# Kernel optimization log

Hardware: AMD Instinct MI355X
Metric: run time of the kernel (lower is better)

Reference implementation:

```python
import jax, jax.numpy as jnp
import numpy as np

N = 40000
E = 640000
D_IN = 128
D_OUT = 128
LN_EPS = 1e-5
LEAKY_ALPHA = 0.2


def setup_inputs() -> dict:
    key = jax.random.key(0)
    ks = jax.random.split(key, 8)
    x = jax.random.normal(ks[0], (N, D_IN), dtype=jnp.float32)
    edge_index = jax.random.randint(ks[1], (2, E), 0, N, dtype=jnp.int64)
    edge_weight = jax.random.uniform(ks[2], (E,), dtype=jnp.float32)
    # learned parameters (kaiming-uniform-ish init for weight)
    bound_w = np.sqrt(6.0 / D_IN) / np.sqrt(1.0 + 5.0)
    weight = jax.random.uniform(ks[3], (D_IN, D_OUT), minval=-bound_w, maxval=bound_w, dtype=jnp.float32)
    adaptive_weight = jax.random.uniform(ks[4], (1,), dtype=jnp.float32)
    bound_b = 1.0 / np.sqrt(D_IN)
    bias = jax.random.uniform(ks[5], (D_OUT,), minval=-bound_b, maxval=bound_b, dtype=jnp.float32)
    ln_gamma = jnp.ones((D_OUT,), dtype=jnp.float32)
    ln_beta = jnp.zeros((D_OUT,), dtype=jnp.float32)
    return {"x": x, "edge_index": edge_index, "edge_weight": edge_weight,
            "weight": weight, "adaptive_weight": adaptive_weight, "bias": bias,
            "ln_gamma": ln_gamma, "ln_beta": ln_beta}


def reference(x, edge_index, edge_weight, weight, adaptive_weight, bias, ln_gamma, ln_beta):
    n = x.shape[0]
    out = x @ weight  # [N, D_OUT]
    row, col = edge_index[0], edge_index[1]
    aew = edge_weight * jax.nn.sigmoid(adaptive_weight[0])  # [E]
    # degree via scatter_add over row
    deg = jax.ops.segment_sum(aew, row, num_segments=n)  # [N]
    deg_inv_sqrt = jnp.where(deg > 0, deg ** -0.5, 0.0)
    norm = deg_inv_sqrt[row] * aew * deg_inv_sqrt[col]  # [E]
    # gather-scale-scatter propagate
    out = jax.ops.segment_sum(out[col] * norm[:, None], row, num_segments=n)  # [N, D_OUT]
    out = out + bias
    # LayerNorm over feature dim
    mu = jnp.mean(out, axis=-1, keepdims=True)
    var = jnp.mean((out - mu) ** 2, axis=-1, keepdims=True)
    out = (out - mu) * jax.lax.rsqrt(var + LN_EPS) * ln_gamma + ln_beta
    # LeakyReLU
    out = jnp.where(out >= 0, out, LEAKY_ALPHA * out)
    return out
```

## Files before the change

kernel.cpp:

```cpp
#include <hip/hip_runtime.h>
#include <hip/hip_bf16.h>
#include <math.h>

#define N_NODES 40000
#define E_EDGES 640000
#define D 128
#define LN_EPS 1e-5f
#define LEAKY 0.2f
#define NB 157

__global__ __launch_bounds__(256) void k_zero(int* __restrict__ cnt) {
    int i = blockIdx.x * 256 + threadIdx.x;
    if (i < N_NODES) cnt[i] = 0;
}

#define BM 32
__global__ __launch_bounds__(256) void k_gemm(const float* __restrict__ x,
                                              const float* __restrict__ w,
                                              float* __restrict__ out) {
    __shared__ float ws[128 * 128];
    __shared__ float xs[BM * 128];
    int t = threadIdx.x;

    const float4* w4 = (const float4*)w;
    float4* ws4 = (float4*)ws;
#pragma unroll
    for (int i = 0; i < 16; i++) ws4[t + i * 256] = w4[t + i * 256];

    int row0 = blockIdx.x * BM;
    const float4* x4 = (const float4*)(x + (size_t)row0 * D);
    float4* xs4 = (float4*)xs;
#pragma unroll
    for (int i = 0; i < 4; i++) xs4[t + i * 256] = x4[t + i * 256];

    __syncthreads();

    int c0 = (t & 31) * 4;
    int r0 = (t >> 5) * 4;
    float acc[4][4] = {};
#pragma unroll 4
    for (int k = 0; k < 128; k++) {
        float4 wv = *(const float4*)&ws[k * 128 + c0];
        float x0 = xs[(r0 + 0) * 128 + k];
        float x1 = xs[(r0 + 1) * 128 + k];
        float x2 = xs[(r0 + 2) * 128 + k];
        float x3 = xs[(r0 + 3) * 128 + k];
        acc[0][0] += x0 * wv.x; acc[0][1] += x0 * wv.y; acc[0][2] += x0 * wv.z; acc[0][3] += x0 * wv.w;
        acc[1][0] += x1 * wv.x; acc[1][1] += x1 * wv.y; acc[1][2] += x1 * wv.z; acc[1][3] += x1 * wv.w;
        acc[2][0] += x2 * wv.x; acc[2][1] += x2 * wv.y; acc[2][2] += x2 * wv.z; acc[2][3] += x2 * wv.w;
        acc[3][0] += x3 * wv.x; acc[3][1] += x3 * wv.y; acc[3][2] += x3 * wv.z; acc[3][3] += x3 * wv.w;
    }
#pragma unroll
    for (int i = 0; i < 4; i++) {
        int row = row0 + r0 + i;
        *(float4*)&out[(size_t)row * D + c0] =
            make_float4(acc[i][0], acc[i][1], acc[i][2], acc[i][3]);
    }
}

__global__ __launch_bounds__(256) void k_cnt(const int* __restrict__ ei,
                                             int* __restrict__ cnt,
                                             int* __restrict__ rank) {
    int e = blockIdx.x * 256 + threadIdx.x;
    if (e >= E_EDGES) return;
    rank[e] = atomicAdd(&cnt[ei[e]], 1);
}

__global__ __launch_bounds__(256) void k_scanA(const int* __restrict__ cnt,
                                               int* __restrict__ bsum) {
    __shared__ int red[256];
    int t = threadIdx.x;
    int i = blockIdx.x * 256 + t;
    red[t] = (i < N_NODES) ? cnt[i] : 0;
    __syncthreads();
    for (int off = 128; off > 0; off >>= 1) {
        if (t < off) red[t] += red[t + off];
        __syncthreads();
    }
    if (t == 0) bsum[blockIdx.x] = red[0];
}

__global__ __launch_bounds__(256) void k_scanB(const int* __restrict__ bsum,
                                               int* __restrict__ boff,
                                               int* __restrict__ rowstart) {
    __shared__ int s[256];
    int t = threadIdx.x;
    int v = (t < NB) ? bsum[t] : 0;
    s[t] = v;
    __syncthreads();
    for (int off = 1; off < 256; off <<= 1) {
        int u = (t >= off) ? s[t - off] : 0;
        __syncthreads();
        s[t] += u;
        __syncthreads();
    }
    if (t < NB) boff[t] = s[t] - v;
    if (t == 0) rowstart[N_NODES] = E_EDGES;
}

__global__ __launch_bounds__(256) void k_scanC(const int* __restrict__ cnt,
                                               const int* __restrict__ boff,
                                               int* __restrict__ rowstart) {
    __shared__ int s[256];
    int t = threadIdx.x;
    int i = blockIdx.x * 256 + t;
    int v = (i < N_NODES) ? cnt[i] : 0;
    s[t] = v;
    __syncthreads();
    for (int off = 1; off < 256; off <<= 1) {
        int u = (t >= off) ? s[t - off] : 0;
        __syncthreads();
        s[t] += u;
        __syncthreads();
    }
    if (i < N_NODES) rowstart[i] = boff[blockIdx.x] + s[t] - v;
}

__global__ __launch_bounds__(256) void k_scat(const int* __restrict__ ei,
                                              const float* __restrict__ ew,
                                              const float* __restrict__ aw,
                                              const int* __restrict__ rowstart,
                                              const int* __restrict__ rank,
                                              float2* __restrict__ srec) {
    int e = blockIdx.x * 256 + threadIdx.x;
    if (e >= E_EDGES) return;
    float sig = 1.f / (1.f + __expf(-aw[0]));
    int r = ei[e];
    int c = ei[E_EDGES + e];
    int slot = rowstart[r] + rank[e];
    srec[slot] = make_float2(__int_as_float(c), ew[e] * sig);
}

__global__ __launch_bounds__(256) void k_degdis(const int* __restrict__ rowstart,
                                                const float2* __restrict__ srec,
                                                float* __restrict__ dis) {
    int i = blockIdx.x * 256 + threadIdx.x;
    if (i >= N_NODES) return;
    int s = rowstart[i];
    int e = rowstart[i + 1];
    float d = 0.f;
    for (int j = s; j < e; j++) d += srec[j].y;
    dis[i] = (d > 0.f) ? rsqrtf(d) : 0.f;
}

__global__ __launch_bounds__(256) void k_agg(const int* __restrict__ rowstart,
                                             const float2* __restrict__ srec,
                                             const float* __restrict__ out_lin,
                                             const float* __restrict__ dis,
                                             const float* __restrict__ bias,
                                             const float* __restrict__ gamma,
                                             const float* __restrict__ beta,
                                             float* __restrict__ out) {
    int w = (blockIdx.x * 256 + threadIdx.x) >> 6;
    int lane = threadIdx.x & 63;
    if (w >= N_NODES) return;
    int s = __builtin_amdgcn_readfirstlane(rowstart[w]);
    int e = __builtin_amdgcn_readfirstlane(rowstart[w + 1]);
    float dr = dis[w];

    float2 acc = make_float2(0.f, 0.f);
    for (int i = s; i < e; i++) {
        float2 rec = srec[i];
        int c = __float_as_int(rec.x);
        float v = rec.y * dis[c];
        const float2 t = *(const float2*)&out_lin[(size_t)c * D + lane * 2];
        acc.x += t.x * v;
        acc.y += t.y * v;
    }
    acc.x *= dr; acc.y *= dr;

    float2 b = *(const float2*)&bias[lane * 2];
    acc.x += b.x; acc.y += b.y;

    float sm = acc.x + acc.y;
#pragma unroll
    for (int m = 1; m < 64; m <<= 1) sm += __shfl_xor(sm, m);
    float mu = sm * (1.f / 128.f);

    float dx = acc.x - mu, dy = acc.y - mu;
    float q = dx * dx + dy * dy;
#pragma unroll
    for (int m = 1; m < 64; m <<= 1) q += __shfl_xor(q, m);
    float rstd = rsqrtf(q * (1.f / 128.f) + LN_EPS);

    float2 g  = *(const float2*)&gamma[lane * 2];
    float2 be = *(const float2*)&beta[lane * 2];
    float y0 = dx * rstd * g.x + be.x;
    float y1 = dy * rstd * g.y + be.y;
    y0 = (y0 >= 0.f) ? y0 : LEAKY * y0;
    y1 = (y1 >= 0.f) ? y1 : LEAKY * y1;
    *(float2*)&out[(size_t)w * D + lane * 2] = make_float2(y0, y1);
}

extern "C" void kernel_launch(void* const* d_in, const int* in_sizes, int n_in,
                              void* d_out, int out_size, void* d_ws, size_t ws_size,
                              hipStream_t stream) {
    const float* x      = (const float*)d_in[0];
    const int*   ei     = (const int*)d_in[1];
    const float* ew     = (const float*)d_in[2];
    const float* w      = (const float*)d_in[3];
    const float* aw     = (const float*)d_in[4];
    const float* bias   = (const float*)d_in[5];
    const float* gamma  = (const float*)d_in[6];
    const float* beta   = (const float*)d_in[7];
    float* out = (float*)d_out;

    char* p = (char*)d_ws;
    float* out_lin  = (float*)p;            p += (size_t)N_NODES * D * 4;
    float* dis      = (float*)p;            p += N_NODES * 4;
    int*   cnt      = (int*)p;              p += N_NODES * 4;
    int*   rowstart = (int*)p;              p += (N_NODES + 1) * 4;
    int*   rank     = (int*)p;              p += (size_t)E_EDGES * 4;
    int*   bsum     = (int*)p;              p += NB * 4;
    int*   boff     = (int*)p;              p += NB * 4;
    float2* srec    = (float2*)((((uintptr_t)p) + 15) & ~(uintptr_t)15);

    k_zero<<<NB, 256, 0, stream>>>(cnt);
    k_gemm<<<N_NODES / BM, 256, 0, stream>>>(x, w, out_lin);
    k_cnt<<<(E_EDGES + 255) / 256, 256, 0, stream>>>(ei, cnt, rank);
    k_scanA<<<NB, 256, 0, stream>>>(cnt, bsum);
    k_scanB<<<1, 256, 0, stream>>>(bsum, boff, rowstart);
    k_scanC<<<NB, 256, 0, stream>>>(cnt, boff, rowstart);
    k_scat<<<(E_EDGES + 255) / 256, 256, 0, stream>>>(ei, ew, aw, rowstart, rank, srec);
    k_degdis<<<NB, 256, 0, stream>>>(rowstart, srec, dis);
    k_agg<<<(N_NODES + 3) / 4, 256, 0, stream>>>(rowstart, srec, out_lin, dis,
                                                 bias, gamma, beta, out);
}
```

Measured before the change: 215.4 us.

## Store linear output in bf16 and fold counter zeroing into GEMM

The GEMM now writes its output as bf16 instead of fp32, which halves the bytes the aggregation kernel gathers per edge from random rows. The separate zeroing kernel is removed and the count zeroing is folded into the GEMM kernel's first threads, saving one launch. This trades precision in the intermediate features (bf16 rounding before accumulation) for lower gather bandwidth, which may affect tolerance.

```diff
diff --git a/kernel.cpp b/kernel.cpp
--- a/kernel.cpp
+++ b/kernel.cpp
@@ -9,15 +9,14 @@
 #define LEAKY 0.2f
 #define NB 157
 
-__global__ __launch_bounds__(256) void k_zero(int* __restrict__ cnt) {
-    int i = blockIdx.x * 256 + threadIdx.x;
-    if (i < N_NODES) cnt[i] = 0;
-}
-
 #define BM 32
 __global__ __launch_bounds__(256) void k_gemm(const float* __restrict__ x,
                                               const float* __restrict__ w,
-                                              float* __restrict__ out) {
+                                              __hip_bfloat16* __restrict__ outb,
+                                              int* __restrict__ cnt) {
+    int gid = blockIdx.x * 256 + threadIdx.x;
+    if (gid < N_NODES) cnt[gid] = 0;
+
     __shared__ float ws[128 * 128];
     __shared__ float xs[BM * 128];
     int t = threadIdx.x;
@@ -53,8 +52,12 @@
 #pragma unroll
     for (int i = 0; i < 4; i++) {
         int row = row0 + r0 + i;
-        *(float4*)&out[(size_t)row * D + c0] =
-            make_float4(acc[i][0], acc[i][1], acc[i][2], acc[i][3]);
+        __hip_bfloat162 p0 = __float22bfloat162_rn(make_float2(acc[i][0], acc[i][1]));
+        __hip_bfloat162 p1 = __float22bfloat162_rn(make_float2(acc[i][2], acc[i][3]));
+        uint2 pk;
+        pk.x = *(unsigned int*)&p0;
+        pk.y = *(unsigned int*)&p1;
+        *(uint2*)&outb[(size_t)row * D + c0] = pk;
     }
 }
 
@@ -145,7 +148,7 @@
 
 __global__ __launch_bounds__(256) void k_agg(const int* __restrict__ rowstart,
                                              const float2* __restrict__ srec,
-                                             const float* __restrict__ out_lin,
+                                             const __hip_bfloat162* __restrict__ lin2,
                                              const float* __restrict__ dis,
                                              const float* __restrict__ bias,
                                              const float* __restrict__ gamma,
@@ -163,9 +166,10 @@
         float2 rec = srec[i];
         int c = __float_as_int(rec.x);
         float v = rec.y * dis[c];
-        const float2 t = *(const float2*)&out_lin[(size_t)c * D + lane * 2];
-        acc.x += t.x * v;
-        acc.y += t.y * v;
+        __hip_bfloat162 t = lin2[(size_t)c * 64 + lane];
+        float2 tf = __bfloat1622float2(t);
+        acc.x += tf.x * v;
+        acc.y += tf.y * v;
     }
     acc.x *= dr; acc.y *= dr;
 
@@ -206,7 +210,7 @@
     float* out = (float*)d_out;
 
     char* p = (char*)d_ws;
-    float* out_lin  = (float*)p;            p += (size_t)N_NODES * D * 4;
+    __hip_bfloat16* out_lin = (__hip_bfloat16*)p; p += (size_t)N_NODES * D * 2;
     float* dis      = (float*)p;            p += N_NODES * 4;
     int*   cnt      = (int*)p;              p += N_NODES * 4;
     int*   rowstart = (int*)p;              p += (N_NODES + 1) * 4;
@@ -215,14 +219,14 @@
     int*   boff     = (int*)p;              p += NB * 4;
     float2* srec    = (float2*)((((uintptr_t)p) + 15) & ~(uintptr_t)15);
 
-    k_zero<<<NB, 256, 0, stream>>>(cnt);
-    k_gemm<<<N_NODES / BM, 256, 0, stream>>>(x, w, out_lin);
+    k_gemm<<<N_NODES / BM, 256, 0, stream>>>(x, w, out_lin, cnt);
     k_cnt<<<(E_EDGES + 255) / 256, 256, 0, stream>>>(ei, cnt, rank);
     k_scanA<<<NB, 256, 0, stream>>>(cnt, bsum);
     k_scanB<<<1, 256, 0, stream>>>(bsum, boff, rowstart);
     k_scanC<<<NB, 256, 0, stream>>>(cnt, boff, rowstart);
     k_scat<<<(E_EDGES + 255) / 256, 256, 0, stream>>>(ei, ew, aw, rowstart, rank, srec);
     k_degdis<<<NB, 256, 0, stream>>>(rowstart, srec, dis);
-    k_agg<<<(N_NODES + 3) / 4, 256, 0, stream>>>(rowstart, srec, out_lin, dis,
+    k_agg<<<(N_NODES + 3) / 4, 256, 0, stream>>>(rowstart, srec,
+                                                 (const __hip_bfloat162*)out_lin, dis,
                                                  bias, gamma, beta, out);
 }
```

Measured after the change: 211.3 us. No clear change (-1.9%).
